# Optimization experiments

Measured on AMD Instinct MI355X. Metric: run time of the kernel, lower is better.

The kernel has to match this reference:

```python
import jax, jax.numpy as jnp
import numpy as np
from jax import lax

N_FREE = 10
DT = 0.1
COMP = 4


def setup_inputs() -> dict:
    key = jax.random.key(0)
    kx, kw = jax.random.split(key)
    B, D = 256, 16384
    nodes = D // COMP  # 4096
    x = jax.random.normal(kx, (B, D), dtype=jnp.float32)
    # Hopfield-style node-coupling matrix (learned parameter), small init for stable relaxation
    W = jax.random.normal(kw, (nodes, nodes), dtype=jnp.float32) * 0.02
    return {"x": x, "W": W}


def reference(x, W):
    B, D = x.shape
    nodes = D // COMP
    # project scalar features to multivectors (B, nodes, comp)
    x_mv = x.reshape(B, nodes, COMP)
    W_sym = 0.5 * (W + W.T)  # symmetric coupling => well-defined energy

    def step(h, _):
        rho = jnp.tanh(h)                                      # (B, nodes, comp)
        drive = jnp.einsum('nm,bmc->bnc', W_sym, rho) + x_mv   # recurrent + input coupling
        grad_E = h - (1.0 - rho * rho) * drive                 # dE/dh
        return h - DT * grad_E, None

    h_free, _ = lax.scan(step, x_mv, None, length=N_FREE)
    return h_free[..., 0]  # scalar (grade-0) component, (B, nodes)
```

## Files before the change

kernel.cpp:

```cpp
#include <hip/hip_runtime.h>
#include <hip/hip_bf16.h>


#define NODES 4096
#define KDIM  4096
#define DLEN  16384
#define BM 64
#define BN 128
#define BK 64
#define NT (KDIM / BK)
#define PSTEP 65536

typedef __attribute__((ext_vector_type(8))) __bf16 bf16x8;
typedef __attribute__((ext_vector_type(4))) float  f32x4;

static __device__ __forceinline__ unsigned short f32_to_bf16(float f) {
    unsigned int u = __float_as_uint(f);
    u += 0x7fffu + ((u >> 16) & 1u);
    return (unsigned short)(u >> 16);
}

__global__ __launch_bounds__(256)
void symw_kernel(const float* __restrict__ W, unsigned short* __restrict__ Wb) {
    __shared__ float Ta[64][64];
    __shared__ float Tb[64][65];
    const int tn = blockIdx.y, tm = blockIdx.x;
    const int c  = threadIdx.x & 63;
    const int r0 = threadIdx.x >> 6;
#pragma unroll
    for (int rr = 0; rr < 16; ++rr) {
        int r = r0 * 16 + rr;
        Ta[r][c] = W[(size_t)(tn * 64 + r) * 4096 + tm * 64 + c];
        Tb[r][c] = W[(size_t)(tm * 64 + r) * 4096 + tn * 64 + c];
    }
    __syncthreads();
#pragma unroll
    for (int rr = 0; rr < 16; ++rr) {
        int r = r0 * 16 + rr;
        float v = 0.5f * (Ta[r][c] + Tb[c][r]);
        Wb[(size_t)(tn * 64 + r) * 4096 + tm * 64 + c] = f32_to_bf16(v);
    }
}

__global__ __launch_bounds__(256)
void init_kernel(const float* __restrict__ x, float* __restrict__ h,
                 unsigned short* __restrict__ P0) {
    int idx = blockIdx.x * blockDim.x + threadIdx.x;
    int b = idx >> 12;
    int m = idx & 4095;
    f32x4 xv = *(const f32x4*)(x + (size_t)idx * 4);
    *(f32x4*)(h + (size_t)idx * 4) = xv;
    size_t base = ((size_t)(m >> 5) * 64 + (b >> 2)) * 512
                + (size_t)((m >> 3) & 3) * 128 + (m & 7);
#pragma unroll
    for (int c = 0; c < 4; ++c) {
        P0[base + (size_t)((b & 3) * 4 + c) * 8] = f32_to_bf16(tanhf(xv[c]));
    }
}

__global__ __launch_bounds__(256, 2)
void step_kernel(const unsigned short* __restrict__ Pcur,
                 const unsigned short* __restrict__ Wb,
                 const float* __restrict__ x,
                 float* __restrict__ h,
                 unsigned short* __restrict__ Pnxt,
                 float* __restrict__ out) {
    __shared__ unsigned short Bs[3][BN * BK];
    __shared__ unsigned short Tp[64][136];

    const int tid  = threadIdx.x;
    const int bx   = blockIdx.x;
    const int by   = blockIdx.y;
    const int rowB0 = bx * BN;

    const int w    = tid >> 6;
    const int lane = tid & 63;
    const int m0   = (w >> 1) * 32;
    const int n0   = (w & 1) * 64;
    const int lr   = lane & 15;
    const int lk   = lane >> 4;
    const int mr0  = by * 4 + (m0 >> 4);

    size_t offB[4];
    int    ldsoB[4];
#pragma unroll
    for (int j = 0; j < 4; ++j) {
        int chunk = tid + 256 * j;
        int row = chunk >> 3, cs = chunk & 7;
        int cg = cs ^ (row & 7);
        offB[j]  = (size_t)(rowB0 + row) * KDIM + cg * 8;
        ldsoB[j] = chunk * 8;
    }
    size_t offa[2][2];
#pragma unroll
    for (int mi = 0; mi < 2; ++mi)
#pragma unroll
        for (int kk = 0; kk < 2; ++kk)
            offa[mi][kk] = (size_t)kk * 32768 + (size_t)(mr0 + mi) * 512 + lane * 8;

    f32x4 acc[2][4];
#pragma unroll
    for (int mi = 0; mi < 2; ++mi)
#pragma unroll
        for (int ni = 0; ni < 4; ++ni)
            acc[mi][ni] = (f32x4){0.f, 0.f, 0.f, 0.f};

    bf16x8 aA[2][2], aB[2][2];
    unsigned short* Bs0 = &Bs[0][0];

#define STAGE(buf, t)                                                           \
    do {                                                                        \
        _Pragma("unroll")                                                       \
        for (int j = 0; j < 4; ++j) {                                           \
            __builtin_amdgcn_global_load_lds(                                   \
                (const __attribute__((address_space(1))) void*)                \
                    (Wb + offB[j] + (size_t)(t) * BK),                          \
                (__attribute__((address_space(3))) void*)                      \
                    (Bs0 + (buf) * (BN * BK) + ldsoB[j]),                       \
                16, 0, 0);                                                      \
        }                                                                       \
    } while (0)

#define LOADA(aset, t)                                                          \
    do {                                                                        \
        const unsigned short* Pt = Pcur + (size_t)(t) * PSTEP;                  \
        _Pragma("unroll")                                                       \
        for (int mi = 0; mi < 2; ++mi)                                          \
            _Pragma("unroll")                                                   \
            for (int kk = 0; kk < 2; ++kk)                                      \
                aset[mi][kk] = *(const bf16x8*)(Pt + offa[mi][kk]);             \
    } while (0)

#define COMPUTE(buf, aset)                                                      \
    do {                                                                        \
        const unsigned short* Bb = Bs0 + (buf) * (BN * BK);                     \
        _Pragma("unroll")                                                       \
        for (int kk = 0; kk < 2; ++kk) {                                        \
            bf16x8 bfr[4];                                                      \
            _Pragma("unroll")                                                   \
            for (int ni = 0; ni < 4; ++ni) {                                    \
                int row = n0 + ni * 16 + lr;                                    \
                int slot = (kk * 4 + lk) ^ (row & 7);                           \
                bfr[ni] = *(const bf16x8*)(Bb + row * BK + slot * 8);           \
            }                                                                   \
            _Pragma("unroll")                                                   \
            for (int mi = 0; mi < 2; ++mi)                                      \
                _Pragma("unroll")                                               \
                for (int ni = 0; ni < 4; ++ni)                                  \
                    acc[mi][ni] = __builtin_amdgcn_mfma_f32_16x16x32_bf16(      \
                        aset[mi][kk], bfr[ni], acc[mi][ni], 0, 0, 0);           \
        }                                                                       \
    } while (0)

    STAGE(0, 0);
    LOADA(aA, 0);
    STAGE(1, 1);
    LOADA(aB, 1);

    int rc = 0, rn = 1, rf = 2;
    for (int tp = 0; tp < 31; ++tp) {
        const int t = tp * 2;
        asm volatile("s_waitcnt vmcnt(8)" ::: "memory");
        __builtin_amdgcn_s_barrier();
        STAGE(rf, t + 2);
        COMPUTE(rc, aA);
        LOADA(aA, t + 2);
        { int z = rc; rc = rn; rn = rf; rf = z; }
        asm volatile("s_waitcnt vmcnt(8)" ::: "memory");
        __builtin_amdgcn_s_barrier();
        STAGE(rf, t + 3);
        COMPUTE(rc, aB);
        LOADA(aB, t + 3);
        { int z = rc; rc = rn; rn = rf; rf = z; }
    }
    asm volatile("s_waitcnt vmcnt(8)" ::: "memory");
    __builtin_amdgcn_s_barrier();
    COMPUTE(rc, aA);
    { int z = rc; rc = rn; rn = rf; rf = z; }
    asm volatile("s_waitcnt vmcnt(0)" ::: "memory");
    __builtin_amdgcn_s_barrier();
    COMPUTE(rc, aB);
#undef STAGE
#undef LOADA
#undef COMPUTE

    const int rowA0 = by * BM;
#pragma unroll
    for (int mi = 0; mi < 2; ++mi) {
        int il = m0 + mi * 16 + lk * 4;
        int i0 = rowA0 + il;
        int b  = i0 >> 2;
#pragma unroll
        for (int ni = 0; ni < 4; ++ni) {
            int nl = n0 + ni * 16 + lr;
            int n  = rowB0 + nl;
            size_t hidx = (size_t)b * DLEN + (size_t)n * 4;
            f32x4 h4 = *(const f32x4*)(h + hidx);
            f32x4 x4 = *(const f32x4*)(x + hidx);
            f32x4 hn;
#pragma unroll
            for (int r = 0; r < 4; ++r) {
                float hv   = h4[r];
                float rho  = tanhf(hv);
                float drive = acc[mi][ni][r] + x4[r];
                float hnew = 0.9f * hv + 0.1f * (1.0f - rho * rho) * drive;
                hn[r] = hnew;
                Tp[il + r][nl] = f32_to_bf16(tanhf(hnew));
            }
            *(f32x4*)(h + hidx) = hn;
            if (out) out[(size_t)b * NODES + n] = hn[0];
        }
    }
    __syncthreads();
#pragma unroll
    for (int q = 0; q < 4; ++q) {
        int chunk = w * 4 + q;
        int kcl = chunk >> 2, mrl = chunk & 3;
        bf16x8 v = *(const bf16x8*)&Tp[mrl * 16 + lr][kcl * 32 + lk * 8];
        size_t po = ((size_t)(bx * 4 + kcl) * 64 + (by * 4 + mrl)) * 512
                  + (size_t)lane * 8;
        *(bf16x8*)(Pnxt + po) = v;
    }
}

extern "C" void kernel_launch(void* const* d_in, const int* in_sizes, int n_in,
                              void* d_out, int out_size, void* d_ws, size_t ws_size,
                              hipStream_t stream) {
    const float* x = (const float*)d_in[0];
    const float* W = (const float*)d_in[1];
    float* out = (float*)d_out;

    char* ws = (char*)d_ws;
    unsigned short* Wb = (unsigned short*)(ws);
    unsigned short* P0 = (unsigned short*)(ws + ((size_t)32 << 20));
    unsigned short* P1 = (unsigned short*)(ws + ((size_t)40 << 20));
    float*          h  = (float*)(ws + ((size_t)48 << 20));

    symw_kernel<<<dim3(64, 64), 256, 0, stream>>>(W, Wb);
    init_kernel<<<dim3(4096), 256, 0, stream>>>(x, h, P0);

    unsigned short* pc = P0;
    unsigned short* pn = P1;
    for (int s = 0; s < 10; ++s) {
        step_kernel<<<dim3(32, 16), 256, 0, stream>>>(
            pc, Wb, x, h, pn, (s == 9) ? out : nullptr);
        unsigned short* t = pc; pc = pn; pn = t;
    }
}
```

Baseline: 611.3 us.

## Split-K the recurrent GEMM into two halves and add a separate combine kernel

The fused step kernel becomes a split-K GEMM. It runs over a 32x16x2 grid with BK=32 and a pre-swizzled MFMA-fragment layout for W, which removes the LDS swizzle math. Each K half writes bf16 partial sums to a workspace, and a new combine kernel adds them, applies the tanh update, and writes the next bf16 activation layout. The goal is to double the block count (512 to 1024) on a 256-CU device and to raise occupancy to 4 blocks per CU. The cost is an extra launch per step, partial-sum traffic through global memory, and added rounding from storing the partials in bf16.

```diff
diff --git a/kernel.cpp b/kernel.cpp
--- a/kernel.cpp
+++ b/kernel.cpp
@@ -4,14 +4,15 @@
 
 #define NODES 4096
 #define KDIM  4096
+#define MDIM  1024
 #define DLEN  16384
 #define BM 64
 #define BN 128
-#define BK 64
-#define NT (KDIM / BK)
-#define PSTEP 65536
+#define BK 32
+#define HALF_ELEMS 4194304
 
 typedef __attribute__((ext_vector_type(8))) __bf16 bf16x8;
+typedef __attribute__((ext_vector_type(8))) unsigned short u16x8;
 typedef __attribute__((ext_vector_type(4))) float  f32x4;
 
 static __device__ __forceinline__ unsigned short f32_to_bf16(float f) {
@@ -19,9 +20,12 @@
     u += 0x7fffu + ((u >> 16) & 1u);
     return (unsigned short)(u >> 16);
 }
+static __device__ __forceinline__ float bf16_to_f32(unsigned short u) {
+    return __uint_as_float(((unsigned int)u) << 16);
+}
 
 __global__ __launch_bounds__(256)
-void symw_kernel(const float* __restrict__ W, unsigned short* __restrict__ Wb) {
+void symw_kernel(const float* __restrict__ W, unsigned short* __restrict__ Wbp) {
     __shared__ float Ta[64][64];
     __shared__ float Tb[64][65];
     const int tn = blockIdx.y, tm = blockIdx.x;
@@ -38,7 +42,11 @@
     for (int rr = 0; rr < 16; ++rr) {
         int r = r0 * 16 + rr;
         float v = 0.5f * (Ta[r][c] + Tb[c][r]);
-        Wb[(size_t)(tn * 64 + r) * 4096 + tm * 64 + c] = f32_to_bf16(v);
+        int n = tn * 64 + r;
+        int k = tm * 64 + c;
+        size_t addr = ((size_t)(k >> 5) * 256 + (n >> 4)) * 512
+                    + (size_t)((n & 15) | (((k >> 3) & 3) << 4)) * 8 + (k & 7);
+        Wbp[addr] = f32_to_bf16(v);
     }
 }
 
@@ -58,45 +66,37 @@
     }
 }
 
-__global__ __launch_bounds__(256, 2)
-void step_kernel(const unsigned short* __restrict__ Pcur,
-                 const unsigned short* __restrict__ Wb,
-                 const float* __restrict__ x,
-                 float* __restrict__ h,
-                 unsigned short* __restrict__ Pnxt,
-                 float* __restrict__ out) {
+__global__ __launch_bounds__(256, 4)
+void gemm_kernel(const unsigned short* __restrict__ Pcur,
+                 const unsigned short* __restrict__ Wbp,
+                 unsigned short* __restrict__ Dp) {
     __shared__ unsigned short Bs[3][BN * BK];
-    __shared__ unsigned short Tp[64][136];
 
     const int tid  = threadIdx.x;
     const int bx   = blockIdx.x;
     const int by   = blockIdx.y;
-    const int rowB0 = bx * BN;
-
+    const int ks   = blockIdx.z;
     const int w    = tid >> 6;
     const int lane = tid & 63;
+    const int lr   = lane & 15;
+    const int lk   = lane >> 4;
     const int m0   = (w >> 1) * 32;
     const int n0   = (w & 1) * 64;
-    const int lr   = lane & 15;
-    const int lk   = lane >> 4;
     const int mr0  = by * 4 + (m0 >> 4);
-
-    size_t offB[4];
-    int    ldsoB[4];
-#pragma unroll
-    for (int j = 0; j < 4; ++j) {
-        int chunk = tid + 256 * j;
-        int row = chunk >> 3, cs = chunk & 7;
-        int cg = cs ^ (row & 7);
-        offB[j]  = (size_t)(rowB0 + row) * KDIM + cg * 8;
-        ldsoB[j] = chunk * 8;
-    }
-    size_t offa[2][2];
+    const int T0   = ks * 64;
+
+    size_t soff[2]; int dsto[2];
+#pragma unroll
+    for (int j = 0; j < 2; ++j) {
+        int c = tid + 256 * j;
+        soff[j] = ((size_t)(bx * 8 + (c >> 6))) * 512 + (size_t)(c & 63) * 8;
+        dsto[j] = c * 8;
+    }
+    size_t aoff[2];
 #pragma unroll
     for (int mi = 0; mi < 2; ++mi)
-#pragma unroll
-        for (int kk = 0; kk < 2; ++kk)
-            offa[mi][kk] = (size_t)kk * 32768 + (size_t)(mr0 + mi) * 512 + lane * 8;
+        aoff[mi] = (size_t)(mr0 + mi) * 512 + (size_t)lane * 8;
+    const int boff = ((w & 1) * 4) * 512 + lane * 8;
 
     f32x4 acc[2][4];
 #pragma unroll
@@ -105,121 +105,139 @@
         for (int ni = 0; ni < 4; ++ni)
             acc[mi][ni] = (f32x4){0.f, 0.f, 0.f, 0.f};
 
-    bf16x8 aA[2][2], aB[2][2];
-    unsigned short* Bs0 = &Bs[0][0];
-
-#define STAGE(buf, t)                                                           \
+    unsigned short* BsF = &Bs[0][0];
+
+#define STAGE(buf, t32)                                                         \
     do {                                                                        \
         _Pragma("unroll")                                                       \
-        for (int j = 0; j < 4; ++j) {                                           \
+        for (int j = 0; j < 2; ++j) {                                           \
             __builtin_amdgcn_global_load_lds(                                   \
                 (const __attribute__((address_space(1))) void*)                \
-                    (Wb + offB[j] + (size_t)(t) * BK),                          \
+                    (Wbp + (size_t)(t32) * 131072 + soff[j]),                   \
                 (__attribute__((address_space(3))) void*)                      \
-                    (Bs0 + (buf) * (BN * BK) + ldsoB[j]),                       \
+                    (BsF + (buf) * 4096 + dsto[j]),                             \
                 16, 0, 0);                                                      \
         }                                                                       \
     } while (0)
 
-#define LOADA(aset, t)                                                          \
+#define LOADA(s, t32)                                                           \
     do {                                                                        \
-        const unsigned short* Pt = Pcur + (size_t)(t) * PSTEP;                  \
+        _Pragma("unroll")                                                       \
+        for (int mi = 0; mi < 2; ++mi)                                          \
+            s[mi] = *(const bf16x8*)(Pcur + (size_t)(t32) * 32768 + aoff[mi]);  \
+    } while (0)
+
+#define COMPUTE(buf, s)                                                         \
+    do {                                                                        \
+        bf16x8 bfr[4];                                                          \
+        _Pragma("unroll")                                                       \
+        for (int ni = 0; ni < 4; ++ni)                                          \
+            bfr[ni] = *(const bf16x8*)(BsF + (buf) * 4096 + boff + ni * 512);   \
         _Pragma("unroll")                                                       \
         for (int mi = 0; mi < 2; ++mi)                                          \
             _Pragma("unroll")                                                   \
-            for (int kk = 0; kk < 2; ++kk)                                      \
-                aset[mi][kk] = *(const bf16x8*)(Pt + offa[mi][kk]);             \
+            for (int ni = 0; ni < 4; ++ni)                                      \
+                acc[mi][ni] = __builtin_amdgcn_mfma_f32_16x16x32_bf16(          \
+                    s[mi], bfr[ni], acc[mi][ni], 0, 0, 0);                      \
     } while (0)
 
-#define COMPUTE(buf, aset)                                                      \
-    do {                                                                        \
-        const unsigned short* Bb = Bs0 + (buf) * (BN * BK);                     \
-        _Pragma("unroll")                                                       \
-        for (int kk = 0; kk < 2; ++kk) {                                        \
-            bf16x8 bfr[4];                                                      \
-            _Pragma("unroll")                                                   \
-            for (int ni = 0; ni < 4; ++ni) {                                    \
-                int row = n0 + ni * 16 + lr;                                    \
-                int slot = (kk * 4 + lk) ^ (row & 7);                           \
-                bfr[ni] = *(const bf16x8*)(Bb + row * BK + slot * 8);           \
-            }                                                                   \
-            _Pragma("unroll")                                                   \
-            for (int mi = 0; mi < 2; ++mi)                                      \
-                _Pragma("unroll")                                               \
-                for (int ni = 0; ni < 4; ++ni)                                  \
-                    acc[mi][ni] = __builtin_amdgcn_mfma_f32_16x16x32_bf16(      \
-                        aset[mi][kk], bfr[ni], acc[mi][ni], 0, 0, 0);           \
-        }                                                                       \
-    } while (0)
-
-    STAGE(0, 0);
-    LOADA(aA, 0);
-    STAGE(1, 1);
-    LOADA(aB, 1);
-
-    int rc = 0, rn = 1, rf = 2;
+    bf16x8 aA[2], aB[2];
+    STAGE(0, T0);     LOADA(aA, T0);
+    STAGE(1, T0 + 1); LOADA(aB, T0 + 1);
+
+    int c0 = 0, c1 = 1, c2 = 2;
     for (int tp = 0; tp < 31; ++tp) {
-        const int t = tp * 2;
-        asm volatile("s_waitcnt vmcnt(8)" ::: "memory");
+        const int t = T0 + 2 * tp;
+        asm volatile("s_waitcnt vmcnt(4)" ::: "memory");
         __builtin_amdgcn_s_barrier();
-        STAGE(rf, t + 2);
-        COMPUTE(rc, aA);
+        STAGE(c2, t + 2);
+        COMPUTE(c0, aA);
         LOADA(aA, t + 2);
-        { int z = rc; rc = rn; rn = rf; rf = z; }
-        asm volatile("s_waitcnt vmcnt(8)" ::: "memory");
+        { int z = c0; c0 = c1; c1 = c2; c2 = z; }
+        asm volatile("s_waitcnt vmcnt(4)" ::: "memory");
         __builtin_amdgcn_s_barrier();
-        STAGE(rf, t + 3);
-        COMPUTE(rc, aB);
+        STAGE(c2, t + 3);
+        COMPUTE(c0, aB);
         LOADA(aB, t + 3);
-        { int z = rc; rc = rn; rn = rf; rf = z; }
-    }
-    asm volatile("s_waitcnt vmcnt(8)" ::: "memory");
+        { int z = c0; c0 = c1; c1 = c2; c2 = z; }
+    }
+    asm volatile("s_waitcnt vmcnt(4)" ::: "memory");
     __builtin_amdgcn_s_barrier();
-    COMPUTE(rc, aA);
-    { int z = rc; rc = rn; rn = rf; rf = z; }
+    COMPUTE(c0, aA);
+    { int z = c0; c0 = c1; c1 = c2; c2 = z; }
     asm volatile("s_waitcnt vmcnt(0)" ::: "memory");
     __builtin_amdgcn_s_barrier();
-    COMPUTE(rc, aB);
+    COMPUTE(c0, aB);
 #undef STAGE
 #undef LOADA
 #undef COMPUTE
 
-    const int rowA0 = by * BM;
+    const int rowA0 = by * BM, rowB0 = bx * BN;
+    unsigned short* D = Dp + (size_t)ks * HALF_ELEMS;
 #pragma unroll
     for (int mi = 0; mi < 2; ++mi) {
-        int il = m0 + mi * 16 + lk * 4;
-        int i0 = rowA0 + il;
-        int b  = i0 >> 2;
+        int i0 = rowA0 + m0 + mi * 16 + lk * 4;
 #pragma unroll
         for (int ni = 0; ni < 4; ++ni) {
-            int nl = n0 + ni * 16 + lr;
-            int n  = rowB0 + nl;
-            size_t hidx = (size_t)b * DLEN + (size_t)n * 4;
-            f32x4 h4 = *(const f32x4*)(h + hidx);
-            f32x4 x4 = *(const f32x4*)(x + hidx);
-            f32x4 hn;
-#pragma unroll
-            for (int r = 0; r < 4; ++r) {
-                float hv   = h4[r];
-                float rho  = tanhf(hv);
-                float drive = acc[mi][ni][r] + x4[r];
-                float hnew = 0.9f * hv + 0.1f * (1.0f - rho * rho) * drive;
-                hn[r] = hnew;
-                Tp[il + r][nl] = f32_to_bf16(tanhf(hnew));
-            }
-            *(f32x4*)(h + hidx) = hn;
-            if (out) out[(size_t)b * NODES + n] = hn[0];
+            int n = rowB0 + n0 + ni * 16 + lr;
+#pragma unroll
+            for (int r = 0; r < 4; ++r)
+                D[(size_t)(i0 + r) * NODES + n] = f32_to_bf16(acc[mi][ni][r]);
         }
     }
-    __syncthreads();
-#pragma unroll
-    for (int q = 0; q < 4; ++q) {
-        int chunk = w * 4 + q;
-        int kcl = chunk >> 2, mrl = chunk & 3;
-        bf16x8 v = *(const bf16x8*)&Tp[mrl * 16 + lr][kcl * 32 + lk * 8];
-        size_t po = ((size_t)(bx * 4 + kcl) * 64 + (by * 4 + mrl)) * 512
-                  + (size_t)lane * 8;
-        *(bf16x8*)(Pnxt + po) = v;
+}
+
+__global__ __launch_bounds__(256)
+void combine_kernel(const unsigned short* __restrict__ Dp,
+                    const float* __restrict__ x,
+                    float* __restrict__ h,
+                    unsigned short* __restrict__ Pnxt,
+                    float* __restrict__ out) {
+    int g  = blockIdx.x * 256 + threadIdx.x;
+    int b  = g >> 9;
+    int mg = (g & 511) << 3;
+    size_t hbase = (size_t)b * DLEN + (size_t)mg * 4;
+
+    f32x4 hv[8], xv[8];
+#pragma unroll
+    for (int e = 0; e < 8; ++e) {
+        hv[e] = *(const f32x4*)(h + hbase + e * 4);
+        xv[e] = *(const f32x4*)(x + hbase + e * 4);
+    }
+    u16x8 d0[4], d1[4];
+#pragma unroll
+    for (int c = 0; c < 4; ++c) {
+        d0[c] = *(const u16x8*)(Dp + (size_t)(b * 4 + c) * NODES + mg);
+        d1[c] = *(const u16x8*)(Dp + HALF_ELEMS + (size_t)(b * 4 + c) * NODES + mg);
+    }
+    u16x8 pn[4];
+    float o[8];
+#pragma unroll
+    for (int e = 0; e < 8; ++e) {
+#pragma unroll
+        for (int c = 0; c < 4; ++c) {
+            float p    = bf16_to_f32(d0[c][e]) + bf16_to_f32(d1[c][e]);
+            float hvv  = hv[e][c];
+            float rho  = tanhf(hvv);
+            float drive = p + xv[e][c];
+            float hnew = 0.9f * hvv + 0.1f * (1.0f - rho * rho) * drive;
+            hv[e][c] = hnew;
+            pn[c][e] = f32_to_bf16(tanhf(hnew));
+            if (c == 0) o[e] = hnew;
+        }
+    }
+#pragma unroll
+    for (int e = 0; e < 8; ++e)
+        *(f32x4*)(h + hbase + e * 4) = hv[e];
+#pragma unroll
+    for (int c = 0; c < 4; ++c) {
+        size_t pa = (size_t)(mg >> 5) * 32768 + (size_t)(b >> 2) * 512
+                  + (size_t)(((b & 3) * 4 + c) | (((mg >> 3) & 3) << 4)) * 8;
+        *(u16x8*)(Pnxt + pa) = pn[c];
+    }
+    if (out) {
+        *(f32x4*)(out + (size_t)b * NODES + mg)     = (f32x4){o[0], o[1], o[2], o[3]};
+        *(f32x4*)(out + (size_t)b * NODES + mg + 4) = (f32x4){o[4], o[5], o[6], o[7]};
     }
 }
 
@@ -231,19 +249,21 @@
     float* out = (float*)d_out;
 
     char* ws = (char*)d_ws;
-    unsigned short* Wb = (unsigned short*)(ws);
-    unsigned short* P0 = (unsigned short*)(ws + ((size_t)32 << 20));
-    unsigned short* P1 = (unsigned short*)(ws + ((size_t)40 << 20));
-    float*          h  = (float*)(ws + ((size_t)48 << 20));
-
-    symw_kernel<<<dim3(64, 64), 256, 0, stream>>>(W, Wb);
+    unsigned short* Wbp = (unsigned short*)(ws);
+    unsigned short* P0  = (unsigned short*)(ws + ((size_t)32 << 20));
+    unsigned short* P1  = (unsigned short*)(ws + ((size_t)40 << 20));
+    float*          h   = (float*)(ws + ((size_t)48 << 20));
+    unsigned short* Dp  = (unsigned short*)(ws + ((size_t)64 << 20));
+
+    symw_kernel<<<dim3(64, 64), 256, 0, stream>>>(W, Wbp);
     init_kernel<<<dim3(4096), 256, 0, stream>>>(x, h, P0);
 
     unsigned short* pc = P0;
     unsigned short* pn = P1;
     for (int s = 0; s < 10; ++s) {
-        step_kernel<<<dim3(32, 16), 256, 0, stream>>>(
-            pc, Wb, x, h, pn, (s == 9) ? out : nullptr);
+        gemm_kernel<<<dim3(32, 16, 2), 256, 0, stream>>>(pc, Wbp, Dp);
+        combine_kernel<<<dim3(512), 256, 0, stream>>>(
+            Dp, x, h, pn, (s == 9) ? out : nullptr);
         unsigned short* t = pc; pc = pn; pn = t;
     }
 }
```

Measured after the change: 648.5 us. 1.06x slower.
